# Optimization experiments

Hardware: AMD Instinct MI355X
Metric: run time of the kernel (lower is better)

Reference implementation:

```python
import jax, jax.numpy as jnp
import numpy as np

HIDDEN, FFN, N_EXPERTS, TOP_K = 1024, 2816, 8, 2


def setup_inputs() -> dict:
    key = jax.random.key(0)
    k1, k2, k3, k4, k5 = jax.random.split(key, 5)
    hidden_states = jax.random.normal(k1, (1, 2048, HIDDEN), dtype=jnp.float32)
    # torch Linear weights: [out, in]; experts stacked on leading E axis
    Wgate = jax.random.normal(k2, (N_EXPERTS, HIDDEN), dtype=jnp.float32) * 0.02
    Wg = jax.random.normal(k3, (N_EXPERTS, FFN, HIDDEN), dtype=jnp.float32) * 0.02
    Wu = jax.random.normal(k4, (N_EXPERTS, FFN, HIDDEN), dtype=jnp.float32) * 0.02
    Wd = jax.random.normal(k5, (N_EXPERTS, HIDDEN, FFN), dtype=jnp.float32) * 0.02
    return {"hidden_states": hidden_states, "Wgate": Wgate, "Wg": Wg, "Wu": Wu, "Wd": Wd}


def reference(hidden_states, Wgate, Wg, Wu, Wd):
    x = hidden_states.reshape(-1, hidden_states.shape[-1])  # [T, H]
    # --- router ---
    logits = jnp.einsum('th,eh->te', x, Wgate)               # [T, E]
    weights = jax.nn.softmax(logits, axis=-1)
    topk_w, topk_i = jax.lax.top_k(weights, TOP_K)           # [T, K]
    topk_w = topk_w / jnp.sum(topk_w, axis=-1, keepdims=True)
    # per-token per-expert combine weight (zero if expert not in top-k)
    comb = jnp.sum(jax.nn.one_hot(topk_i, N_EXPERTS, dtype=x.dtype) * topk_w[..., None], axis=1)  # [T, E]
    # --- all-expert SwiGLU (dense reference for the gather-compute-scatter loop) ---
    g = jnp.einsum('th,efh->tef', x, Wg)                     # [T, E, F]
    u = jnp.einsum('th,efh->tef', x, Wu)
    h = jax.nn.silu(g) * u
    y = jnp.einsum('tef,ehf->teh', h, Wd)                    # [T, E, H]
    out = jnp.einsum('te,teh->th', comb, y)                  # [T, H]
    return out
```

## Files before the change

kernel.cpp:

```cpp
#include <hip/hip_runtime.h>
#include <hip/hip_bf16.h>

#define HIDDEN 1024
#define FFN    2816
#define NEXP   8
#define NTOK   2048

typedef __attribute__((ext_vector_type(8))) short short8;
typedef __attribute__((ext_vector_type(4))) short bf16x4;
typedef __attribute__((ext_vector_type(4))) float f32x4;

static __device__ __forceinline__ short f2bf(float f) {
    __hip_bfloat16 h = __float2bfloat16(f);
    return *(short*)&h;
}

static __device__ __forceinline__ void gl_lds16(const short* g, short* l) {
    __builtin_amdgcn_global_load_lds(
        (const __attribute__((address_space(1))) void*)g,
        (__attribute__((address_space(3))) void*)l, 16, 0, 0);
}

#define WAITV(N) asm volatile("s_waitcnt vmcnt(" #N ")" ::: "memory")
#define LGKM0    asm volatile("s_waitcnt lgkmcnt(0)" ::: "memory")
#define BAR()    do { __builtin_amdgcn_s_barrier(); \
                      __builtin_amdgcn_sched_barrier(0); } while (0)

static __device__ __forceinline__ void
router_body(int t, int lane, const float* __restrict__ x,
            const float* __restrict__ Wgate, int* __restrict__ counts,
            int* __restrict__ tok, float* __restrict__ wts)
{
    float acc[NEXP];
#pragma unroll
    for (int e = 0; e < NEXP; e++) acc[e] = 0.f;
    const float* xrow = x + (size_t)t * HIDDEN;
    for (int h = lane; h < HIDDEN; h += 64) {
        float xv = xrow[h];
#pragma unroll
        for (int e = 0; e < NEXP; e++) acc[e] += xv * Wgate[e * HIDDEN + h];
    }
#pragma unroll
    for (int off = 32; off > 0; off >>= 1) {
#pragma unroll
        for (int e = 0; e < NEXP; e++) acc[e] += __shfl_down(acc[e], off);
    }
    if (lane == 0) {
        float mx = acc[0];
#pragma unroll
        for (int e = 1; e < NEXP; e++) mx = fmaxf(mx, acc[e]);
        float p[NEXP];
#pragma unroll
        for (int e = 0; e < NEXP; e++) p[e] = __expf(acc[e] - mx);
        int i0 = 0; float p0 = p[0];
#pragma unroll
        for (int e = 1; e < NEXP; e++) if (p[e] > p0) { p0 = p[e]; i0 = e; }
        int i1 = -1; float p1 = -1.f;
#pragma unroll
        for (int e = 0; e < NEXP; e++) {
            if (e == i0) continue;
            if (p[e] > p1) { p1 = p[e]; i1 = e; }
        }
        float inv = 1.f / (p0 + p1);
        float w0 = p0 * inv, w1 = p1 * inv;
        int s0 = atomicAdd(&counts[i0], 1);
        tok[i0 * NTOK + s0] = t; wts[i0 * NTOK + s0] = w0;
        int s1 = atomicAdd(&counts[i1], 1);
        tok[i1 * NTOK + s1] = t; wts[i1 * NTOK + s1] = w1;
    }
}

__global__ void __launch_bounds__(64)
router_kernel(const float* __restrict__ x, const float* __restrict__ Wgate,
              int* __restrict__ counts, int* __restrict__ tok,
              float* __restrict__ wts)
{
    router_body(blockIdx.x, threadIdx.x, x, Wgate, counts, tok, wts);
}

__global__ void __launch_bounds__(256)
fused_rxz(const float* __restrict__ x, const float* __restrict__ Wgate,
          int* __restrict__ counts, int* __restrict__ tok,
          float* __restrict__ wts, short* __restrict__ xbf,
          float* __restrict__ out)
{
    int bid = blockIdx.x;
    int tid = threadIdx.x;
    if (bid < 512) {
        router_body(bid * 4 + (tid >> 6), tid & 63, x, Wgate, counts, tok, wts);
        return;
    }
    if (bid < 1024) {
        long long base4 = (long long)(bid - 512) * 1024;
#pragma unroll
        for (int p = 0; p < 4; p++) {
            long long r = base4 + p * 256 + tid;
            float4 a = ((const float4*)x)[r];
            bf16x4 o;
            o[0] = f2bf(a.x); o[1] = f2bf(a.y); o[2] = f2bf(a.z); o[3] = f2bf(a.w);
            *(bf16x4*)(xbf + 4 * r) = o;
        }
        return;
    }
    long long base4 = (long long)(bid - 1024) * 1024;
    float4 z = make_float4(0.f, 0.f, 0.f, 0.f);
#pragma unroll
    for (int p = 0; p < 4; p++)
        ((float4*)out)[base4 + p * 256 + tid] = z;
}

#define FFN1_BLOCKS 2816
#define CVTD_BLOCKS 2048
__global__ void __launch_bounds__(256, 2)
ffn1_v7(const short* __restrict__ xbf, const float* __restrict__ Wg,
        const float* __restrict__ Wu, const int* __restrict__ counts,
        const int* __restrict__ tok, short* __restrict__ hbuf,
        const float* __restrict__ Wd, short* __restrict__ wdbf)
{
    int bid = blockIdx.x;
    int tid = threadIdx.x;
    if (bid >= FFN1_BLOCKS) {
        long long base4 = (long long)(bid - FFN1_BLOCKS) * 2816;
#pragma unroll
        for (int p = 0; p < 11; p++) {
            long long r = base4 + p * 256 + tid;
            float4 a = ((const float4*)Wd)[r];
            bf16x4 o;
            o[0] = f2bf(a.x); o[1] = f2bf(a.y); o[2] = f2bf(a.z); o[3] = f2bf(a.w);
            *(bf16x4*)(wdbf + 4 * r) = o;
        }
        return;
    }
    int xb  = bid / 176;
    int yz  = bid - xb * 176;
    int e   = yz / 22;
    int fb  = yz - e * 22;
    int cnt = counts[e];
    int row0 = xb * 128;
    if (row0 >= cnt) return;
    int off_e = 0;
#pragma unroll
    for (int i = 0; i < NEXP; i++) if (i < e) off_e += counts[i];
    int f0 = fb * 128;

    __shared__ short Xs[2][128 * 32];
    __shared__ short Gs[2][128 * 32];
    __shared__ short Us[2][128 * 32];
    __shared__ int   stok[128];

    if (tid < 128) stok[tid] = tok[e * NTOK + min(row0 + tid, cnt - 1)];
    __syncthreads();

    int lane = tid & 63, w = tid >> 6;
    int l15 = lane & 15, lq = lane >> 4;
    int wm = (w & 1) * 64, wn = (w >> 1) * 64;

    int prow   = lane >> 2;
    int gchunk = (lane & 3) ^ ((lane >> 3) & 3);
    const short* xsrc[2]; const float* gsrc[2]; const float* usrc[2];
    int rb[2];
#pragma unroll
    for (int j = 0; j < 2; j++) {
        int rbase = w * 32 + j * 16;
        int r = rbase + prow;
        xsrc[j] = xbf + (size_t)stok[r] * HIDDEN + gchunk * 8;
        gsrc[j] = Wg + (size_t)e * FFN * HIDDEN + (size_t)(f0 + r) * HIDDEN + gchunk * 8;
        usrc[j] = Wu + (size_t)e * FFN * HIDDEN + (size_t)(f0 + r) * HIDDEN + gchunk * 8;
        rb[j] = rbase * 32;
    }
    int wadr0 = rb[0] + lane * 8;
    int wadr1 = rb[1] + lane * 8;

    int aoff[4], boff[4];
#pragma unroll
    for (int mi = 0; mi < 4; mi++) {
        int r = wm + mi * 16 + l15;
        aoff[mi] = r * 32 + (lq ^ ((r >> 1) & 3)) * 8;
    }
#pragma unroll
    for (int ni = 0; ni < 4; ni++) {
        int r = wn + ni * 16 + l15;
        boff[ni] = r * 32 + (lq ^ ((r >> 1) & 3)) * 8;
    }

    f32x4 cg[4][4], cu[4][4];
#pragma unroll
    for (int i = 0; i < 4; i++)
#pragma unroll
        for (int j = 0; j < 4; j++) { cg[i][j] = (f32x4)0.f; cu[i][j] = (f32x4)0.f; }

    float4 g0a, g0b, g1a, g1b, u0a, u0b, u1a, u1b;

#define XDMA(B, T) do { int _k = (T) * 32;                          \
    gl_lds16(xsrc[0] + _k, &Xs[B][rb[0]]);                          \
    gl_lds16(xsrc[1] + _k, &Xs[B][rb[1]]); } while (0)

#define LOADR(T) do { int _k = (T) * 32;                            \
    g0a = *(const float4*)(gsrc[0] + _k);                           \
    g0b = *(const float4*)(gsrc[0] + _k + 4);                       \
    g1a = *(const float4*)(gsrc[1] + _k);                           \
    g1b = *(const float4*)(gsrc[1] + _k + 4);                       \
    u0a = *(const float4*)(usrc[0] + _k);                           \
    u0b = *(const float4*)(usrc[0] + _k + 4);                       \
    u1a = *(const float4*)(usrc[1] + _k);                           \
    u1b = *(const float4*)(usrc[1] + _k + 4); } while (0)

#define PK8(dst, A, Bv) do { short8 _o;                             \
    _o[0] = f2bf(A.x);  _o[1] = f2bf(A.y);                          \
    _o[2] = f2bf(A.z);  _o[3] = f2bf(A.w);                          \
    _o[4] = f2bf(Bv.x); _o[5] = f2bf(Bv.y);                         \
    _o[6] = f2bf(Bv.z); _o[7] = f2bf(Bv.w);                         \
    *(short8*)(dst) = _o; } while (0)

#define CVTW(B) do {                                                \
    PK8(&Gs[B][wadr0], g0a, g0b); PK8(&Gs[B][wadr1], g1a, g1b);     \
    PK8(&Us[B][wadr0], u0a, u0b); PK8(&Us[B][wadr1], u1a, u1b); } while (0)

#define COMP1(B) do {                                               \
    short8 af[4];                                                   \
    _Pragma("unroll")                                               \
    for (int mi = 0; mi < 4; mi++)                                  \
        af[mi] = *(const short8*)&Xs[B][aoff[mi]];                  \
    {   short8 bb[4];                                               \
        _Pragma("unroll")                                           \
        for (int ni = 0; ni < 4; ni++)                              \
            bb[ni] = *(const short8*)&Gs[B][boff[ni]];              \
        _Pragma("unroll")                                           \
        for (int mi = 0; mi < 4; mi++)                              \
        _Pragma("unroll")                                           \
        for (int ni = 0; ni < 4; ni++)                              \
            cg[mi][ni] = __builtin_amdgcn_mfma_f32_16x16x32_bf16(af[mi], bb[ni], cg[mi][ni], 0, 0, 0); \
    }                                                               \
    {   short8 bb[4];                                               \
        _Pragma("unroll")                                           \
        for (int ni = 0; ni < 4; ni++)                              \
            bb[ni] = *(const short8*)&Us[B][boff[ni]];              \
        _Pragma("unroll")                                           \
        for (int mi = 0; mi < 4; mi++)                              \
        _Pragma("unroll")                                           \
        for (int ni = 0; ni < 4; ni++)                              \
            cu[mi][ni] = __builtin_amdgcn_mfma_f32_16x16x32_bf16(af[mi], bb[ni], cu[mi][ni], 0, 0, 0); \
    } } while (0)

    XDMA(0, 0); LOADR(0);

    for (int tt = 0; tt < 32; tt += 2) {
        CVTW(0);
        XDMA(1, tt + 1); LOADR(tt + 1);
        WAITV(10); LGKM0; BAR();
        COMP1(0);
        BAR();
        CVTW(1);
        if (tt + 2 < 32) {
            XDMA(0, tt + 2); LOADR(tt + 2);
            WAITV(10);
        } else {
            WAITV(0);
        }
        LGKM0; BAR();
        COMP1(1);
        BAR();
    }

#undef XDMA
#undef LOADR
#undef PK8
#undef CVTW
#undef COMP1

#pragma unroll
    for (int mi = 0; mi < 4; mi++)
#pragma unroll
        for (int r = 0; r < 4; r++) {
            int row = wm + mi * 16 + lq * 4 + r;
            int grow = row0 + row;
            if (grow < cnt) {
                short* hrow = hbuf + (size_t)(off_e + grow) * FFN + f0 + wn;
#pragma unroll
                for (int ni = 0; ni < 4; ni++) {
                    float g = cg[mi][ni][r], u = cu[mi][ni][r];
                    float h = g / (1.f + __expf(-g)) * u;
                    hrow[ni * 16 + l15] = f2bf(h);
                }
            }
        }
}

__global__ void __launch_bounds__(256, 2)
ffn2_v6(const short* __restrict__ hbuf, const short* __restrict__ Wdbf,
        const int* __restrict__ counts, const int* __restrict__ tok,
        const float* __restrict__ wts, float* __restrict__ out)
{
    int bid = blockIdx.x;
    int xb  = bid >> 7;
    int yz  = bid & 127;
    int e   = yz >> 4;
    int y   = yz & 15;
    int cnt = counts[e];
    int row0 = xb * 128;
    if (row0 >= cnt) return;
    int off_e = 0;
#pragma unroll
    for (int i = 0; i < NEXP; i++) if (i < e) off_e += counts[i];
    int h0    = (y >> 1) * 128;
    int kbase = (y & 1) * (FFN / 2);

    __shared__ short Hs[3][128 * 32];
    __shared__ short Ds[3][128 * 32];
    __shared__ int   stok[128];
    __shared__ float swt[128];

    int tid = threadIdx.x;
    if (tid < 128) {
        int rc = min(row0 + tid, cnt - 1);
        stok[tid] = tok[e * NTOK + rc];
        swt[tid]  = wts[e * NTOK + rc];
    }
    __syncthreads();

    int lane = tid & 63, w = tid >> 6;
    int l15 = lane & 15, lq = lane >> 4;
    int wm = (w & 1) * 64, wn = (w >> 1) * 64;

    int prow   = lane >> 2;
    int gchunk = (lane & 3) ^ ((lane >> 3) & 3);
    const short* hsrc[2]; const short* dsrc[2];
    int rb[2];
#pragma unroll
    for (int j = 0; j < 2; j++) {
        int rbase = w * 32 + j * 16;
        int r = rbase + prow;
        hsrc[j] = hbuf + (size_t)(off_e + min(row0 + r, cnt - 1)) * FFN + kbase + gchunk * 8;
        dsrc[j] = Wdbf + (size_t)e * HIDDEN * FFN + (size_t)(h0 + r) * FFN + kbase + gchunk * 8;
        rb[j] = rbase * 32;
    }

    int aoff[4], boff[4];
#pragma unroll
    for (int mi = 0; mi < 4; mi++) {
        int r = wm + mi * 16 + l15;
        aoff[mi] = r * 32 + (lq ^ ((r >> 1) & 3)) * 8;
    }
#pragma unroll
    for (int ni = 0; ni < 4; ni++) {
        int r = wn + ni * 16 + l15;
        boff[ni] = r * 32 + (lq ^ ((r >> 1) & 3)) * 8;
    }

    f32x4 c[4][4];
#pragma unroll
    for (int i = 0; i < 4; i++)
#pragma unroll
        for (int j = 0; j < 4; j++) c[i][j] = (f32x4)0.f;

#define STAGE2(B, T) do { int _k = (T) * 32;                       \
    _Pragma("unroll")                                              \
    for (int j = 0; j < 2; j++) {                                  \
        gl_lds16(hsrc[j] + _k, &Hs[B][rb[j]]);                     \
        gl_lds16(dsrc[j] + _k, &Ds[B][rb[j]]);                     \
    } } while (0)

#define COMP2(B) do {                                              \
    short8 af[4], bd[4];                                           \
    _Pragma("unroll")                                              \
    for (int mi = 0; mi < 4; mi++)                                 \
        af[mi] = *(const short8*)&Hs[B][aoff[mi]];                 \
    _Pragma("unroll")                                              \
    for (int ni = 0; ni < 4; ni++)                                 \
        bd[ni] = *(const short8*)&Ds[B][boff[ni]];                 \
    _Pragma("unroll")                                              \
    for (int mi = 0; mi < 4; mi++)                                 \
    _Pragma("unroll")                                              \
    for (int ni = 0; ni < 4; ni++)                                 \
        c[mi][ni] = __builtin_amdgcn_mfma_f32_16x16x32_bf16(af[mi], bd[ni], c[mi][ni], 0, 0, 0); \
    } while (0)

    STAGE2(0, 0); STAGE2(1, 1); STAGE2(2, 2);

    for (int tt = 0; tt < 42; tt += 3) {
        WAITV(8); BAR(); COMP2(0); BAR(); STAGE2(0, tt + 3);
        WAITV(8); BAR(); COMP2(1); BAR(); STAGE2(1, tt + 4);
        WAITV(8); BAR(); COMP2(2); BAR(); if (tt + 5 < 44) STAGE2(2, tt + 5);
    }
    WAITV(4); BAR(); COMP2(0);
    WAITV(0); BAR(); COMP2(1);

#undef STAGE2
#undef COMP2

#pragma unroll
    for (int mi = 0; mi < 4; mi++)
#pragma unroll
        for (int r = 0; r < 4; r++) {
            int row = wm + mi * 16 + lq * 4 + r;
            int grow = row0 + row;
            if (grow < cnt) {
                int t = stok[row];
                float wgt = swt[row];
                float* orow = out + (size_t)t * HIDDEN + h0 + wn;
#pragma unroll
                for (int ni = 0; ni < 4; ni++)
                    atomicAdd(&orow[ni * 16 + l15], wgt * c[mi][ni][r]);
            }
        }
}

#define LDW 40
__global__ void __launch_bounds__(256, 2)
ffn1_fb(const float* __restrict__ x, const float* __restrict__ Wg,
        const float* __restrict__ Wu, const int* __restrict__ counts,
        const int* __restrict__ tok, __hip_bfloat16* __restrict__ hbuf)
{
    int e = blockIdx.z;
    int cnt = counts[e];
    int row0 = blockIdx.x * 128;
    if (row0 >= cnt) return;
    int off_e = 0;
#pragma unroll
    for (int i = 0; i < NEXP; i++) if (i < e) off_e += counts[i];
    int f0 = blockIdx.y * 64;

    __shared__ short Xs[128][LDW];
    __shared__ short Gs[64][LDW];
    __shared__ short Us[64][LDW];
    __shared__ int   stok[128];

    int tid = threadIdx.x;
    if (tid < 128) stok[tid] = tok[e * NTOK + min(row0 + tid, cnt - 1)];
    __syncthreads();

    int lane = tid & 63, w = tid >> 6;
    int wm = (w & 1) * 64, wn = (w >> 1) * 32;
    int l15 = lane & 15, lq = lane >> 4;

    f32x4 cg[4][2], cu[4][2];
#pragma unroll
    for (int i = 0; i < 4; i++)
#pragma unroll
        for (int j = 0; j < 2; j++) { cg[i][j] = (f32x4)0.f; cu[i][j] = (f32x4)0.f; }

    const float* Wge = Wg + (size_t)e * FFN * HIDDEN;
    const float* Wue = Wu + (size_t)e * FFN * HIDDEN;

    int xr[4], xc[4]; const float* xp[4];
#pragma unroll
    for (int i = 0; i < 4; i++) {
        int idx = tid + 256 * i;
        xr[i] = idx >> 3; xc[i] = (idx & 7) * 4;
        xp[i] = x + (size_t)stok[xr[i]] * HIDDEN + xc[i];
    }
    int wr[2], wc[2]; const float* gp[2]; const float* up[2];
#pragma unroll
    for (int i = 0; i < 2; i++) {
        int idx = tid + 256 * i;
        wr[i] = idx >> 3; wc[i] = (idx & 7) * 4;
        gp[i] = Wge + (size_t)(f0 + wr[i]) * HIDDEN + wc[i];
        up[i] = Wue + (size_t)(f0 + wr[i]) * HIDDEN + wc[i];
    }

    float4 xa[4], ga[2], ua[2];
#pragma unroll
    for (int i = 0; i < 4; i++) xa[i] = *(const float4*)(xp[i]);
#pragma unroll
    for (int i = 0; i < 2; i++) { ga[i] = *(const float4*)(gp[i]); ua[i] = *(const float4*)(up[i]); }

    for (int k0 = 0; k0 < HIDDEN; k0 += 32) {
        __syncthreads();
#pragma unroll
        for (int i = 0; i < 4; i++) {
            short* d = &Xs[xr[i]][xc[i]];
            d[0] = f2bf(xa[i].x); d[1] = f2bf(xa[i].y);
            d[2] = f2bf(xa[i].z); d[3] = f2bf(xa[i].w);
        }
#pragma unroll
        for (int i = 0; i < 2; i++) {
            short* d = &Gs[wr[i]][wc[i]];
            d[0] = f2bf(ga[i].x); d[1] = f2bf(ga[i].y);
            d[2] = f2bf(ga[i].z); d[3] = f2bf(ga[i].w);
            short* d2 = &Us[wr[i]][wc[i]];
            d2[0] = f2bf(ua[i].x); d2[1] = f2bf(ua[i].y);
            d2[2] = f2bf(ua[i].z); d2[3] = f2bf(ua[i].w);
        }
        __syncthreads();
        if (k0 + 32 < HIDDEN) {
            int kn = k0 + 32;
#pragma unroll
            for (int i = 0; i < 4; i++) xa[i] = *(const float4*)(xp[i] + kn);
#pragma unroll
            for (int i = 0; i < 2; i++) { ga[i] = *(const float4*)(gp[i] + kn); ua[i] = *(const float4*)(up[i] + kn); }
        }
        short8 af[4], bg[2], bu[2];
#pragma unroll
        for (int mi = 0; mi < 4; mi++) af[mi] = *(const short8*)&Xs[wm + mi * 16 + l15][lq * 8];
#pragma unroll
        for (int ni = 0; ni < 2; ni++) {
            bg[ni] = *(const short8*)&Gs[wn + ni * 16 + l15][lq * 8];
            bu[ni] = *(const short8*)&Us[wn + ni * 16 + l15][lq * 8];
        }
#pragma unroll
        for (int mi = 0; mi < 4; mi++)
#pragma unroll
            for (int ni = 0; ni < 2; ni++) {
                cg[mi][ni] = __builtin_amdgcn_mfma_f32_16x16x32_bf16(af[mi], bg[ni], cg[mi][ni], 0, 0, 0);
                cu[mi][ni] = __builtin_amdgcn_mfma_f32_16x16x32_bf16(af[mi], bu[ni], cu[mi][ni], 0, 0, 0);
            }
    }

#pragma unroll
    for (int mi = 0; mi < 4; mi++)
#pragma unroll
        for (int r = 0; r < 4; r++) {
            int row = wm + mi * 16 + lq * 4 + r;
            int grow = row0 + row;
            if (grow < cnt) {
                __hip_bfloat16* hrow = hbuf + (size_t)(off_e + grow) * FFN + f0 + wn;
#pragma unroll
                for (int ni = 0; ni < 2; ni++) {
                    float g = cg[mi][ni][r], u = cu[mi][ni][r];
                    float h = g / (1.f + __expf(-g)) * u;
                    hrow[ni * 16 + l15] = __float2bfloat16(h);
                }
            }
        }
}

__global__ void __launch_bounds__(256, 2)
ffn2_fb(const __hip_bfloat16* __restrict__ hbuf, const float* __restrict__ Wd,
        const int* __restrict__ counts, const int* __restrict__ tok,
        const float* __restrict__ wts, float* __restrict__ out)
{
    int e = blockIdx.z;
    int cnt = counts[e];
    int row0 = blockIdx.x * 128;
    if (row0 >= cnt) return;
    int off_e = 0;
#pragma unroll
    for (int i = 0; i < NEXP; i++) if (i < e) off_e += counts[i];
    int h0 = blockIdx.y * 64;

    __shared__ short Hs[128][LDW];
    __shared__ short Ds[64][LDW];
    __shared__ int   stok[128];
    __shared__ float swt[128];

    int tid = threadIdx.x;
    if (tid < 128) {
        int rc = min(row0 + tid, cnt - 1);
        stok[tid] = tok[e * NTOK + rc];
        swt[tid]  = wts[e * NTOK + rc];
    }
    __syncthreads();

    int lane = tid & 63, w = tid >> 6;
    int wm = (w & 1) * 64, wn = (w >> 1) * 32;
    int l15 = lane & 15, lq = lane >> 4;

    f32x4 c[4][2];
#pragma unroll
    for (int i = 0; i < 4; i++)
#pragma unroll
        for (int j = 0; j < 2; j++) c[i][j] = (f32x4)0.f;

    const float* Wde = Wd + (size_t)e * HIDDEN * FFN;

    int hr[2], hc[2]; const short* hp[2];
#pragma unroll
    for (int i = 0; i < 2; i++) {
        int idx = tid + 256 * i;
        hr[i] = idx >> 2; hc[i] = (idx & 3) * 8;
        int ar = min(row0 + hr[i], cnt - 1);
        hp[i] = (const short*)(hbuf + (size_t)(off_e + ar) * FFN + hc[i]);
    }
    int dr[2], dc[2]; const float* dp[2];
#pragma unroll
    for (int i = 0; i < 2; i++) {
        int idx = tid + 256 * i;
        dr[i] = idx >> 3; dc[i] = (idx & 7) * 4;
        dp[i] = Wde + (size_t)(h0 + dr[i]) * FFN + dc[i];
    }

    short8 ha[2]; float4 da[2];
#pragma unroll
    for (int i = 0; i < 2; i++) { ha[i] = *(const short8*)(hp[i]); da[i] = *(const float4*)(dp[i]); }

    for (int k0 = 0; k0 < FFN; k0 += 32) {
        __syncthreads();
#pragma unroll
        for (int i = 0; i < 2; i++) {
            *(short8*)&Hs[hr[i]][hc[i]] = ha[i];
            short* d = &Ds[dr[i]][dc[i]];
            d[0] = f2bf(da[i].x); d[1] = f2bf(da[i].y);
            d[2] = f2bf(da[i].z); d[3] = f2bf(da[i].w);
        }
        __syncthreads();
        if (k0 + 32 < FFN) {
            int kn = k0 + 32;
#pragma unroll
            for (int i = 0; i < 2; i++) { ha[i] = *(const short8*)(hp[i] + kn); da[i] = *(const float4*)(dp[i] + kn); }
        }
        short8 af[4], bf_[2];
#pragma unroll
        for (int mi = 0; mi < 4; mi++) af[mi] = *(const short8*)&Hs[wm + mi * 16 + l15][lq * 8];
#pragma unroll
        for (int ni = 0; ni < 2; ni++) bf_[ni] = *(const short8*)&Ds[wn + ni * 16 + l15][lq * 8];
#pragma unroll
        for (int mi = 0; mi < 4; mi++)
#pragma unroll
            for (int ni = 0; ni < 2; ni++)
                c[mi][ni] = __builtin_amdgcn_mfma_f32_16x16x32_bf16(af[mi], bf_[ni], c[mi][ni], 0, 0, 0);
    }

#pragma unroll
    for (int mi = 0; mi < 4; mi++)
#pragma unroll
        for (int r = 0; r < 4; r++) {
            int row = wm + mi * 16 + lq * 4 + r;
            int grow = row0 + row;
            if (grow < cnt) {
                int t = stok[row];
                float wgt = swt[row];
                float* orow = out + (size_t)t * HIDDEN + h0 + wn;
#pragma unroll
                for (int ni = 0; ni < 2; ni++)
                    atomicAdd(&orow[ni * 16 + l15], wgt * c[mi][ni][r]);
            }
        }
}

extern "C" void kernel_launch(void* const* d_in, const int* in_sizes, int n_in,
                              void* d_out, int out_size, void* d_ws, size_t ws_size,
                              hipStream_t stream) {
    const float* x     = (const float*)d_in[0];
    const float* Wgate = (const float*)d_in[1];
    const float* Wg    = (const float*)d_in[2];
    const float* Wu    = (const float*)d_in[3];
    const float* Wd    = (const float*)d_in[4];
    float* out = (float*)d_out;

    char* ws = (char*)d_ws;
    int*   counts = (int*)ws;
    int*   tok    = (int*)(ws + 256);
    float* wts    = (float*)(ws + 256 + NEXP * NTOK * 4);

    hipMemsetAsync(counts, 0, 256, stream);

    const size_t base = 256 + 2 * (size_t)NEXP * NTOK * 4;
    const size_t NEED = base
        + 2ull * NTOK * HIDDEN
        + 2ull * NEXP * HIDDEN * FFN
        + 2ull * 2ull * NTOK * FFN;

    if (ws_size >= NEED) {
        short* xbf  = (short*)(ws + base);
        short* wdbf = xbf  + (size_t)NTOK * HIDDEN;
        short* hbuf = wdbf + (size_t)NEXP * HIDDEN * FFN;

        fused_rxz<<<1536, 256, 0, stream>>>(x, Wgate, counts, tok, wts, xbf, out);

        ffn1_v7<<<FFN1_BLOCKS + CVTD_BLOCKS, 256, 0, stream>>>(
            xbf, Wg, Wu, counts, tok, hbuf, Wd, wdbf);

        ffn2_v6<<<2048, 256, 0, stream>>>(hbuf, wdbf, counts, tok, wts, out);
    } else {
        hipMemsetAsync(out, 0, (size_t)out_size * sizeof(float), stream);
        router_kernel<<<NTOK, 64, 0, stream>>>(x, Wgate, counts, tok, wts);
        __hip_bfloat16* hbuf = (__hip_bfloat16*)(ws + base);
        dim3 g1(NTOK / 128, FFN / 64, NEXP);
        ffn1_fb<<<g1, 256, 0, stream>>>(x, Wg, Wu, counts, tok, hbuf);
        dim3 g2(NTOK / 128, HIDDEN / 64, NEXP);
        ffn2_fb<<<g2, 256, 0, stream>>>(hbuf, Wd, counts, tok, wts, out);
    }
}
```

Measured before the change: 457.3 us.

## Deepen FFN1 weight prefetch to two register sets for two-tile lookahead

The FFN1 kernel now keeps two register sets for fp32 gate/up weight tiles, so global loads for tile t+2 and t+3 are issued a full compute phase before they are converted and written to LDS. Before, each tile was loaded only one step ahead. The aim is to hide more global-memory latency behind the MFMA work. The second register set raises VGPR pressure under launch_bounds(256,2), which could cause spills or lower occupancy. The vmcnt wait counts also have to match the new load ordering.

```diff
diff --git a/kernel.cpp b/kernel.cpp
--- a/kernel.cpp
+++ b/kernel.cpp
@@ -112,7 +112,7 @@
 #define FFN1_BLOCKS 2816
 #define CVTD_BLOCKS 2048
 __global__ void __launch_bounds__(256, 2)
-ffn1_v7(const short* __restrict__ xbf, const float* __restrict__ Wg,
+ffn1_v8(const short* __restrict__ xbf, const float* __restrict__ Wg,
         const float* __restrict__ Wu, const int* __restrict__ counts,
         const int* __restrict__ tok, short* __restrict__ hbuf,
         const float* __restrict__ Wd, short* __restrict__ wdbf)
@@ -189,21 +189,32 @@
 #pragma unroll
         for (int j = 0; j < 4; j++) { cg[i][j] = (f32x4)0.f; cu[i][j] = (f32x4)0.f; }
 
-    float4 g0a, g0b, g1a, g1b, u0a, u0b, u1a, u1b;
+    float4 Ag0a, Ag0b, Ag1a, Ag1b, Au0a, Au0b, Au1a, Au1b;
+    float4 Bg0a, Bg0b, Bg1a, Bg1b, Bu0a, Bu0b, Bu1a, Bu1b;
 
 #define XDMA(B, T) do { int _k = (T) * 32;                          \
     gl_lds16(xsrc[0] + _k, &Xs[B][rb[0]]);                          \
     gl_lds16(xsrc[1] + _k, &Xs[B][rb[1]]); } while (0)
 
-#define LOADR(T) do { int _k = (T) * 32;                            \
-    g0a = *(const float4*)(gsrc[0] + _k);                           \
-    g0b = *(const float4*)(gsrc[0] + _k + 4);                       \
-    g1a = *(const float4*)(gsrc[1] + _k);                           \
-    g1b = *(const float4*)(gsrc[1] + _k + 4);                       \
-    u0a = *(const float4*)(usrc[0] + _k);                           \
-    u0b = *(const float4*)(usrc[0] + _k + 4);                       \
-    u1a = *(const float4*)(usrc[1] + _k);                           \
-    u1b = *(const float4*)(usrc[1] + _k + 4); } while (0)
+#define LOADR_A(T) do { int _k = (T) * 32;                          \
+    Ag0a = *(const float4*)(gsrc[0] + _k);                          \
+    Ag0b = *(const float4*)(gsrc[0] + _k + 4);                      \
+    Ag1a = *(const float4*)(gsrc[1] + _k);                          \
+    Ag1b = *(const float4*)(gsrc[1] + _k + 4);                      \
+    Au0a = *(const float4*)(usrc[0] + _k);                          \
+    Au0b = *(const float4*)(usrc[0] + _k + 4);                      \
+    Au1a = *(const float4*)(usrc[1] + _k);                          \
+    Au1b = *(const float4*)(usrc[1] + _k + 4); } while (0)
+
+#define LOADR_B(T) do { int _k = (T) * 32;                          \
+    Bg0a = *(const float4*)(gsrc[0] + _k);                          \
+    Bg0b = *(const float4*)(gsrc[0] + _k + 4);                      \
+    Bg1a = *(const float4*)(gsrc[1] + _k);                          \
+    Bg1b = *(const float4*)(gsrc[1] + _k + 4);                      \
+    Bu0a = *(const float4*)(usrc[0] + _k);                          \
+    Bu0b = *(const float4*)(usrc[0] + _k + 4);                      \
+    Bu1a = *(const float4*)(usrc[1] + _k);                          \
+    Bu1b = *(const float4*)(usrc[1] + _k + 4); } while (0)
 
 #define PK8(dst, A, Bv) do { short8 _o;                             \
     _o[0] = f2bf(A.x);  _o[1] = f2bf(A.y);                          \
@@ -212,9 +223,13 @@
     _o[6] = f2bf(Bv.z); _o[7] = f2bf(Bv.w);                         \
     *(short8*)(dst) = _o; } while (0)
 
-#define CVTW(B) do {                                                \
-    PK8(&Gs[B][wadr0], g0a, g0b); PK8(&Gs[B][wadr1], g1a, g1b);     \
-    PK8(&Us[B][wadr0], u0a, u0b); PK8(&Us[B][wadr1], u1a, u1b); } while (0)
+#define CVTW_A() do {                                               \
+    PK8(&Gs[0][wadr0], Ag0a, Ag0b); PK8(&Gs[0][wadr1], Ag1a, Ag1b); \
+    PK8(&Us[0][wadr0], Au0a, Au0b); PK8(&Us[0][wadr1], Au1a, Au1b); } while (0)
+
+#define CVTW_B() do {                                               \
+    PK8(&Gs[1][wadr0], Bg0a, Bg0b); PK8(&Gs[1][wadr1], Bg1a, Bg1b); \
+    PK8(&Us[1][wadr0], Bu0a, Bu0b); PK8(&Us[1][wadr1], Bu1a, Bu1b); } while (0)
 
 #define COMP1(B) do {                                               \
     short8 af[4];                                                   \
@@ -242,30 +257,28 @@
             cu[mi][ni] = __builtin_amdgcn_mfma_f32_16x16x32_bf16(af[mi], bb[ni], cu[mi][ni], 0, 0, 0); \
     } } while (0)
 
-    XDMA(0, 0); LOADR(0);
+    LOADR_A(0); XDMA(0, 0);
+    LOADR_B(1); XDMA(1, 1);
 
     for (int tt = 0; tt < 32; tt += 2) {
-        CVTW(0);
-        XDMA(1, tt + 1); LOADR(tt + 1);
-        WAITV(10); LGKM0; BAR();
+        WAITV(10);
+        CVTW_A(); LGKM0; BAR();
         COMP1(0);
         BAR();
-        CVTW(1);
-        if (tt + 2 < 32) {
-            XDMA(0, tt + 2); LOADR(tt + 2);
-            WAITV(10);
-        } else {
-            WAITV(0);
-        }
-        LGKM0; BAR();
+        if (tt + 2 < 32) { LOADR_A(tt + 2); XDMA(0, tt + 2); WAITV(10); }
+        else             { WAITV(0); }
+        CVTW_B(); LGKM0; BAR();
         COMP1(1);
         BAR();
+        if (tt + 3 < 32) { LOADR_B(tt + 3); XDMA(1, tt + 3); }
     }
 
 #undef XDMA
-#undef LOADR
+#undef LOADR_A
+#undef LOADR_B
 #undef PK8
-#undef CVTW
+#undef CVTW_A
+#undef CVTW_B
 #undef COMP1
 
 #pragma unroll
@@ -657,7 +670,7 @@
 
         fused_rxz<<<1536, 256, 0, stream>>>(x, Wgate, counts, tok, wts, xbf, out);
 
-        ffn1_v7<<<FFN1_BLOCKS + CVTD_BLOCKS, 256, 0, stream>>>(
+        ffn1_v8<<<FFN1_BLOCKS + CVTD_BLOCKS, 256, 0, stream>>>(
             xbf, Wg, Wu, counts, tok, hbuf, Wd, wdbf);
 
         ffn2_v6<<<2048, 256, 0, stream>>>(hbuf, wdbf, counts, tok, wts, out);
```

Result: slower. 486.4 us (+6.3%).

## Convert Wd to bf16 inside FFN2 loads instead of a separate pre-pass

Applied to the files above, without the earlier changes.

Removes the standalone Wd fp32-to-bf16 conversion blocks from the FFN1 launch and the bf16 Wd workspace buffer. FFN2 now loads fp32 Wd through registers and packs it to bf16 into LDS inside its main loop, the same way FFN1 handles Wg/Wu. The pipeline goes from triple-buffered async LDS loads to double buffering with register staging. This avoids writing and re-reading a converted Wd copy, at the cost of more global bytes per FFN2 block, since Wd tiles are re-read as fp32 by every token-row block, and less latency hiding.

```diff
diff --git a/kernel.cpp b/kernel.cpp
--- a/kernel.cpp
+++ b/kernel.cpp
@@ -110,27 +110,13 @@
 }
 
 #define FFN1_BLOCKS 2816
-#define CVTD_BLOCKS 2048
 __global__ void __launch_bounds__(256, 2)
-ffn1_v7(const short* __restrict__ xbf, const float* __restrict__ Wg,
-        const float* __restrict__ Wu, const int* __restrict__ counts,
-        const int* __restrict__ tok, short* __restrict__ hbuf,
-        const float* __restrict__ Wd, short* __restrict__ wdbf)
+ffn1_v10(const short* __restrict__ xbf, const float* __restrict__ Wg,
+         const float* __restrict__ Wu, const int* __restrict__ counts,
+         const int* __restrict__ tok, short* __restrict__ hbuf)
 {
     int bid = blockIdx.x;
     int tid = threadIdx.x;
-    if (bid >= FFN1_BLOCKS) {
-        long long base4 = (long long)(bid - FFN1_BLOCKS) * 2816;
-#pragma unroll
-        for (int p = 0; p < 11; p++) {
-            long long r = base4 + p * 256 + tid;
-            float4 a = ((const float4*)Wd)[r];
-            bf16x4 o;
-            o[0] = f2bf(a.x); o[1] = f2bf(a.y); o[2] = f2bf(a.z); o[3] = f2bf(a.w);
-            *(bf16x4*)(wdbf + 4 * r) = o;
-        }
-        return;
-    }
     int xb  = bid / 176;
     int yz  = bid - xb * 176;
     int e   = yz / 22;
@@ -251,12 +237,8 @@
         COMP1(0);
         BAR();
         CVTW(1);
-        if (tt + 2 < 32) {
-            XDMA(0, tt + 2); LOADR(tt + 2);
-            WAITV(10);
-        } else {
-            WAITV(0);
-        }
+        if (tt + 2 < 32) { XDMA(0, tt + 2); LOADR(tt + 2); WAITV(10); }
+        else             { WAITV(0); }
         LGKM0; BAR();
         COMP1(1);
         BAR();
@@ -264,7 +246,6 @@
 
 #undef XDMA
 #undef LOADR
-#undef PK8
 #undef CVTW
 #undef COMP1
 
@@ -287,7 +268,7 @@
 }
 
 __global__ void __launch_bounds__(256, 2)
-ffn2_v6(const short* __restrict__ hbuf, const short* __restrict__ Wdbf,
+ffn2_v9(const short* __restrict__ hbuf, const float* __restrict__ Wd,
         const int* __restrict__ counts, const int* __restrict__ tok,
         const float* __restrict__ wts, float* __restrict__ out)
 {
@@ -305,8 +286,8 @@
     int h0    = (y >> 1) * 128;
     int kbase = (y & 1) * (FFN / 2);
 
-    __shared__ short Hs[3][128 * 32];
-    __shared__ short Ds[3][128 * 32];
+    __shared__ short Hs[2][128 * 32];
+    __shared__ short Ds[2][128 * 32];
     __shared__ int   stok[128];
     __shared__ float swt[128];
 
@@ -324,16 +305,18 @@
 
     int prow   = lane >> 2;
     int gchunk = (lane & 3) ^ ((lane >> 3) & 3);
-    const short* hsrc[2]; const short* dsrc[2];
+    const short* hsrc[2]; const float* dsrc[2];
     int rb[2];
 #pragma unroll
     for (int j = 0; j < 2; j++) {
         int rbase = w * 32 + j * 16;
         int r = rbase + prow;
         hsrc[j] = hbuf + (size_t)(off_e + min(row0 + r, cnt - 1)) * FFN + kbase + gchunk * 8;
-        dsrc[j] = Wdbf + (size_t)e * HIDDEN * FFN + (size_t)(h0 + r) * FFN + kbase + gchunk * 8;
+        dsrc[j] = Wd + (size_t)e * HIDDEN * FFN + (size_t)(h0 + r) * FFN + kbase + gchunk * 8;
         rb[j] = rbase * 32;
     }
+    int wadr0 = rb[0] + lane * 8;
+    int wadr1 = rb[1] + lane * 8;
 
     int aoff[4], boff[4];
 #pragma unroll
@@ -353,40 +336,57 @@
 #pragma unroll
         for (int j = 0; j < 4; j++) c[i][j] = (f32x4)0.f;
 
-#define STAGE2(B, T) do { int _k = (T) * 32;                       \
-    _Pragma("unroll")                                              \
-    for (int j = 0; j < 2; j++) {                                  \
-        gl_lds16(hsrc[j] + _k, &Hs[B][rb[j]]);                     \
-        gl_lds16(dsrc[j] + _k, &Ds[B][rb[j]]);                     \
-    } } while (0)
-
-#define COMP2(B) do {                                              \
-    short8 af[4], bd[4];                                           \
-    _Pragma("unroll")                                              \
-    for (int mi = 0; mi < 4; mi++)                                 \
-        af[mi] = *(const short8*)&Hs[B][aoff[mi]];                 \
-    _Pragma("unroll")                                              \
-    for (int ni = 0; ni < 4; ni++)                                 \
-        bd[ni] = *(const short8*)&Ds[B][boff[ni]];                 \
-    _Pragma("unroll")                                              \
-    for (int mi = 0; mi < 4; mi++)                                 \
-    _Pragma("unroll")                                              \
-    for (int ni = 0; ni < 4; ni++)                                 \
+    float4 d0a, d0b, d1a, d1b;
+
+#define HDMA(B, T) do { int _k = (T) * 32;                          \
+    gl_lds16(hsrc[0] + _k, &Hs[B][rb[0]]);                          \
+    gl_lds16(hsrc[1] + _k, &Hs[B][rb[1]]); } while (0)
+
+#define LOADD(T) do { int _k = (T) * 32;                            \
+    d0a = *(const float4*)(dsrc[0] + _k);                           \
+    d0b = *(const float4*)(dsrc[0] + _k + 4);                       \
+    d1a = *(const float4*)(dsrc[1] + _k);                           \
+    d1b = *(const float4*)(dsrc[1] + _k + 4); } while (0)
+
+#define CVTD(B) do {                                                \
+    PK8(&Ds[B][wadr0], d0a, d0b); PK8(&Ds[B][wadr1], d1a, d1b); } while (0)
+
+#define COMP2(B) do {                                               \
+    short8 af[4], bd[4];                                            \
+    _Pragma("unroll")                                               \
+    for (int mi = 0; mi < 4; mi++)                                  \
+        af[mi] = *(const short8*)&Hs[B][aoff[mi]];                  \
+    _Pragma("unroll")                                               \
+    for (int ni = 0; ni < 4; ni++)                                  \
+        bd[ni] = *(const short8*)&Ds[B][boff[ni]];                  \
+    _Pragma("unroll")                                               \
+    for (int mi = 0; mi < 4; mi++)                                  \
+    _Pragma("unroll")                                               \
+    for (int ni = 0; ni < 4; ni++)                                  \
         c[mi][ni] = __builtin_amdgcn_mfma_f32_16x16x32_bf16(af[mi], bd[ni], c[mi][ni], 0, 0, 0); \
     } while (0)
 
-    STAGE2(0, 0); STAGE2(1, 1); STAGE2(2, 2);
-
-    for (int tt = 0; tt < 42; tt += 3) {
-        WAITV(8); BAR(); COMP2(0); BAR(); STAGE2(0, tt + 3);
-        WAITV(8); BAR(); COMP2(1); BAR(); STAGE2(1, tt + 4);
-        WAITV(8); BAR(); COMP2(2); BAR(); if (tt + 5 < 44) STAGE2(2, tt + 5);
-    }
-    WAITV(4); BAR(); COMP2(0);
-    WAITV(0); BAR(); COMP2(1);
-
-#undef STAGE2
+    HDMA(0, 0); LOADD(0);
+
+    for (int tt = 0; tt < 44; tt += 2) {
+        CVTD(0);
+        HDMA(1, tt + 1); LOADD(tt + 1);
+        WAITV(6); LGKM0; BAR();
+        COMP2(0);
+        BAR();
+        CVTD(1);
+        if (tt + 2 < 44) { HDMA(0, tt + 2); LOADD(tt + 2); WAITV(6); }
+        else             { WAITV(0); }
+        LGKM0; BAR();
+        COMP2(1);
+        BAR();
+    }
+
+#undef HDMA
+#undef LOADD
+#undef CVTD
 #undef COMP2
+#undef PK8
 
 #pragma unroll
     for (int mi = 0; mi < 4; mi++)
@@ -647,20 +647,17 @@
     const size_t base = 256 + 2 * (size_t)NEXP * NTOK * 4;
     const size_t NEED = base
         + 2ull * NTOK * HIDDEN
-        + 2ull * NEXP * HIDDEN * FFN
         + 2ull * 2ull * NTOK * FFN;
 
     if (ws_size >= NEED) {
         short* xbf  = (short*)(ws + base);
-        short* wdbf = xbf  + (size_t)NTOK * HIDDEN;
-        short* hbuf = wdbf + (size_t)NEXP * HIDDEN * FFN;
+        short* hbuf = xbf + (size_t)NTOK * HIDDEN;
 
         fused_rxz<<<1536, 256, 0, stream>>>(x, Wgate, counts, tok, wts, xbf, out);
 
-        ffn1_v7<<<FFN1_BLOCKS + CVTD_BLOCKS, 256, 0, stream>>>(
-            xbf, Wg, Wu, counts, tok, hbuf, Wd, wdbf);
-
-        ffn2_v6<<<2048, 256, 0, stream>>>(hbuf, wdbf, counts, tok, wts, out);
+        ffn1_v10<<<FFN1_BLOCKS, 256, 0, stream>>>(xbf, Wg, Wu, counts, tok, hbuf);
+
+        ffn2_v9<<<2048, 256, 0, stream>>>(hbuf, Wd, counts, tok, wts, out);
     } else {
         hipMemsetAsync(out, 0, (size_t)out_size * sizeof(float), stream);
         router_kernel<<<NTOK, 64, 0, stream>>>(x, Wgate, counts, tok, wts);
```

Result: faster. 447.0 us (-2.2%).
